# Optimization experiments

Measured on AMD Instinct MI355X. Metric: run time of the kernel, lower is better.

The kernel has to match this reference:

```python
import math
import jax, jax.numpy as jnp
import numpy as np

B, S, HID = 2, 2048, 1024
NH, DQ, DV = 16, 64, 64

def _alibi_bias(n_heads, maxlen):
    # standard ALiBi slopes: 2^(-8*(h+1)/n_heads)
    slopes = jnp.asarray([2.0 ** (-8.0 * (h + 1) / n_heads) for h in range(n_heads)], dtype=jnp.float32)
    pos = jnp.arange(maxlen, dtype=jnp.float32)
    rel = pos[None, :] - pos[:, None]              # [i, j] = j - i  (<= 0 on causal part)
    return slopes[:, None, None] * rel[None]       # [n_heads, maxlen, maxlen]

def setup_inputs() -> dict:
    key = jax.random.key(0)
    ks = jax.random.split(key, 6)
    scale = 0.02
    return {
        "hidden_states": jax.random.normal(ks[0], (B, S, HID), dtype=jnp.float32),
        "attention_mask": jnp.ones((B, S), dtype=jnp.int32),
        "Wq": jax.random.normal(ks[1], (HID, NH * DQ), dtype=jnp.float32) * scale,
        "Wk": jax.random.normal(ks[2], (HID, NH * DQ), dtype=jnp.float32) * scale,
        "Wv": jax.random.normal(ks[3], (HID, NH * DV), dtype=jnp.float32) * scale,
        "Wo": jax.random.normal(ks[4], (NH * DV, HID), dtype=jnp.float32) * scale,
        "bo": jnp.zeros((HID,), dtype=jnp.float32),
        "alibi": _alibi_bias(NH, S),
    }

def reference(hidden_states, attention_mask, Wq, Wk, Wv, Wo, bo, alibi):
    N, t, _ = hidden_states.shape
    # QKV projections (no bias), split into heads: [N, H, t, d]
    q = (hidden_states @ Wq).reshape(N, t, NH, DQ).transpose(0, 2, 1, 3)
    k = (hidden_states @ Wk).reshape(N, t, NH, DQ).transpose(0, 2, 1, 3)
    v = (hidden_states @ Wv).reshape(N, t, NH, DV).transpose(0, 2, 1, 3)
    # raw scores, then ALiBi added BEFORE the 1/sqrt(d) scaling (as in source)
    scores = jnp.einsum("bhid,bhjd->bhij", q, k)
    scores = scores + alibi[None, :, :t, :t]
    scores = scores / math.sqrt(DQ)
    # grok tanh softcap at 30
    scores = 30.0 * jnp.tanh(scores / 30.0)
    # causal + padding masks
    causal = jnp.tril(jnp.ones((t, t), dtype=bool))
    scores = jnp.where(causal[None, None], scores, -jnp.inf)
    pad = (attention_mask != 0)[:, None, None, :]  # [N,1,1,T]
    scores = jnp.where(pad, scores, -jnp.inf)
    probs = jax.nn.softmax(scores, axis=-1)        # dropout p=0.0 (eval)
    ctx = jnp.einsum("bhij,bhjd->bhid", probs, v)
    ctx = ctx.transpose(0, 2, 1, 3).reshape(N, t, NH * DV)
    out = ctx @ Wo + bo
    return out
```

## Files before the change

kernel.cpp:

```cpp
#include <hip/hip_runtime.h>
#include <hip/hip_bf16.h>
#include <stdint.h>

#define BB 2
#define SS 2048
#define HID 1024
#define NHEAD 16
#define DHEAD 64
#define MTOT (BB*SS)

typedef float  f32x4  __attribute__((ext_vector_type(4)));
typedef short  s16x8  __attribute__((ext_vector_type(8)));
typedef unsigned short u16x4 __attribute__((ext_vector_type(4)));

#define LOG2E 1.4426950408889634f

__device__ __forceinline__ unsigned short f2bf(float x){
  union { float f; unsigned u; } v; v.f = x;
  unsigned r = v.u + 0x7fffu + ((v.u >> 16) & 1u);
  return (unsigned short)(r >> 16);
}
__device__ __forceinline__ unsigned pk2bf(float a, float b){
  __hip_bfloat162 h = __float22bfloat162_rn(make_float2(a, b));
  union { __hip_bfloat162 h; unsigned u; } v; v.h = h; return v.u;
}
__device__ __forceinline__ float bf2f(unsigned short h){
  union { unsigned u; float f; } v; v.u = ((unsigned)h) << 16; return v.f;
}

__device__ __forceinline__ void gl2lds16(const unsigned short* g, unsigned short* l){
  __builtin_amdgcn_global_load_lds((const __attribute__((address_space(1))) void*)g,
                                   (__attribute__((address_space(3))) void*)l, 16, 0, 0);
}

__global__ __launch_bounds__(256) void k_convert_x(const float* __restrict__ x,
                                                   unsigned short* __restrict__ xb){
  int i = blockIdx.x * 256 + threadIdx.x;
  const float4* xp = (const float4*)x;
  float4 v = xp[i];
  uint2 o; o.x = pk2bf(v.x, v.y); o.y = pk2bf(v.z, v.w);
  ((uint2*)xb)[i] = o;
}

__global__ __launch_bounds__(256) void k_convert_w(const float* __restrict__ Wq,
                                                   const float* __restrict__ Wk,
                                                   const float* __restrict__ Wv,
                                                   const float* __restrict__ Wo,
                                                   unsigned short* __restrict__ Wt,
                                                   unsigned short* __restrict__ Wot){
  __shared__ float tile[64][65];
  int z = blockIdx.z;
  const float* src = (z==0) ? Wq : (z==1) ? Wk : (z==2) ? Wv : Wo;
  unsigned short* dst = (z < 3) ? (Wt + z * HID * HID) : Wot;
  int n0 = blockIdx.x * 64, k0 = blockIdx.y * 64;
  int t = threadIdx.x, tx = t & 63, ty = t >> 6;
  #pragma unroll
  for (int i = 0; i < 16; i++){
    int kl = ty + i*4;
    tile[kl][tx] = src[(k0 + kl) * HID + n0 + tx];
  }
  __syncthreads();
  #pragma unroll
  for (int i = 0; i < 16; i++){
    int nl = ty + i*4;
    dst[(n0 + nl) * HID + k0 + tx] = f2bf(tile[tx][nl]);
  }
}

__global__ __launch_bounds__(256) void k_gemm_qkv(const unsigned short* __restrict__ A,
                                                  const unsigned short* __restrict__ Bt,
                                                  unsigned short* __restrict__ Qb,
                                                  unsigned short* __restrict__ Kb,
                                                  unsigned short* __restrict__ Vb){
  __shared__ __align__(16) unsigned short As[128*32];
  __shared__ __align__(16) unsigned short Bs[128*32];
  int t = threadIdx.x;
  int L = t & 63, w = t >> 6;
  int q = L >> 4, c = L & 15;
  int id = blockIdx.x;
  int xcd = id & 7, pos = id >> 3;
  int m0 = (xcd*4 + (pos & 3)) * 128;
  int n0 = (pos >> 2) * 128;
  int wr = w >> 1, wc = w & 1;
  f32x4 acc[4][4];
  #pragma unroll
  for (int i = 0; i < 4; i++)
    #pragma unroll
    for (int j = 0; j < 4; j++) acc[i][j] = (f32x4){0.f,0.f,0.f,0.f};

  for (int kb = 0; kb < 32; kb++){
    __syncthreads();
    #pragma unroll
    for (int i = 0; i < 2; i++){
      int p = t + i*256;
      int row = p >> 2, cp = p & 3;
      gl2lds16(A  + (m0 + row) * HID + kb*32 + cp*8, As + p*8);
      gl2lds16(Bt + (n0 + row) * HID + kb*32 + cp*8, Bs + p*8);
    }
    __syncthreads();
    s16x8 af[4], bf[4];
    #pragma unroll
    for (int i = 0; i < 4; i++){
      int m = wr*64 + i*16 + c;
      af[i] = *(const s16x8*)(As + m*32 + q*8);
      int n = wc*64 + i*16 + c;
      bf[i] = *(const s16x8*)(Bs + n*32 + q*8);
    }
    #pragma unroll
    for (int i = 0; i < 4; i++)
      #pragma unroll
      for (int j = 0; j < 4; j++)
        acc[i][j] = __builtin_amdgcn_mfma_f32_16x16x32_bf16(af[i], bf[j], acc[i][j], 0, 0, 0);
  }

  int wsel = n0 >> 10;
  unsigned short* dst = (wsel==0) ? Qb : (wsel==1) ? Kb : Vb;
  float scale = (wsel==0) ? 0.125f : 1.0f;
  #pragma unroll
  for (int i = 0; i < 4; i++){
    #pragma unroll
    for (int j = 0; j < 4; j++){
      int m_l = wr*64 + i*16 + q*4;
      int nw  = (n0 + wc*64 + j*16 + c) & 1023;
      unsigned ua = pk2bf(acc[i][j][0]*scale, acc[i][j][1]*scale);
      unsigned ub = pk2bf(acc[i][j][2]*scale, acc[i][j][3]*scale);
      dst[(m0 + m_l + 0) * HID + nw] = (unsigned short)ua;
      dst[(m0 + m_l + 1) * HID + nw] = (unsigned short)(ua >> 16);
      dst[(m0 + m_l + 2) * HID + nw] = (unsigned short)ub;
      dst[(m0 + m_l + 3) * HID + nw] = (unsigned short)(ub >> 16);
    }
  }
}

__global__ __launch_bounds__(256) void k_transpose_v(const unsigned short* __restrict__ Vb,
                                                     unsigned short* __restrict__ Vt){
  __shared__ unsigned tile[64][33];
  int st = blockIdx.x, bh = blockIdx.y;
  int b = bh >> 4, h = bh & 15;
  int t = threadIdx.x;
  int lr = t >> 4, lc = t & 15;
  #pragma unroll
  for (int i = 0; i < 4; i++){
    int sl = lr + i*16;
    u16x4 v = *(const u16x4*)(Vb + (size_t)(b*SS + st*64 + sl) * HID + h*DHEAD + lc*4);
    tile[sl][lc*2]     = (unsigned)v.x | ((unsigned)v.y << 16);
    tile[sl][lc*2 + 1] = (unsigned)v.z | ((unsigned)v.w << 16);
  }
  __syncthreads();
  #pragma unroll
  for (int i = 0; i < 4; i++){
    int dl = lr + i*16;
    int sh = (dl & 1) * 16, dw = dl >> 1;
    u16x4 o;
    o.x = (unsigned short)(tile[lc*4 + 0][dw] >> sh);
    o.y = (unsigned short)(tile[lc*4 + 1][dw] >> sh);
    o.z = (unsigned short)(tile[lc*4 + 2][dw] >> sh);
    o.w = (unsigned short)(tile[lc*4 + 3][dw] >> sh);
    *(u16x4*)(Vt + (size_t)(bh*DHEAD + dl) * SS + st*64 + lc*4) = o;
  }
}

__global__ __launch_bounds__(256) void k_attn(const unsigned short* __restrict__ Qb,
                                              const unsigned short* __restrict__ Kb,
                                              const unsigned short* __restrict__ Vt,
                                              const int* __restrict__ amask,
                                              unsigned short* __restrict__ NumBf,
                                              float* __restrict__ Lsum,
                                              float* __restrict__ Part2,
                                              float* __restrict__ L2){
  __shared__ __align__(16) unsigned short UQ[4*16*72];
  __shared__ __align__(16) unsigned short Ks[64*64];
  __shared__ __align__(16) unsigned short Vs[64*64];

  int t = threadIdx.x;
  int L = t & 63, w = t >> 6;
  int q = L >> 4, c = L & 15;
  int x = blockIdx.x;
  int bh = blockIdx.y;
  int b = bh >> 4, h = bh & 15;

  int qt, ci, nc;
  if (x < 24){        qt = 31 - x/3;           ci = x % 3;       nc = 3; }
  else if (x < 48){   int y = x - 24; qt = 23 - y/2; ci = y & 1; nc = 2; }
  else {              qt = 59 - x;             ci = 0;           nc = 1; }
  int i0 = qt * 64;

  int hp = h + 1;
  float slope = (hp & 1) ? 0.70710678118654752f : 1.0f;
  slope = ldexpf(slope, -((hp >> 1) + 3));

  int Di = (int)(15.0f / slope);
  int dd = i0 - Di;
  int jt_lo = dd > 0 ? (dd >> 6) : 0;
  int nt = qt + 1 - jt_lo;
  int jt0 = jt_lo + (nt * ci) / nc;
  int jt1 = jt_lo + (nt * (ci + 1)) / nc;

  #pragma unroll
  for (int i = 0; i < 2; i++){
    int p = t + i*256; int row = p >> 3, cp = p & 7; int gc = cp ^ (row & 7);
    gl2lds16(Qb + (size_t)(b*SS + i0 + row) * HID + h*DHEAD + gc*8, UQ + p*8);
  }
  __syncthreads();
  s16x8 qf0, qf1;
  {
    int m = w*16 + c;
    qf0 = *(const s16x8*)(UQ + m*64 + ((0 + q) ^ (m & 7)) * 8);
    qf1 = *(const s16x8*)(UQ + m*64 + ((4 + q) ^ (m & 7)) * 8);
  }

  float si[4];
  #pragma unroll
  for (int r = 0; r < 4; r++) si[r] = slope * (float)(i0 + w*16 + q*4 + r);

  f32x4 cacc[4];
  #pragma unroll
  for (int i = 0; i < 4; i++) cacc[i] = (f32x4){0.f,0.f,0.f,0.f};
  float lrow[4] = {0.f,0.f,0.f,0.f};

  const float C1 = 86.5617024533378f;
  const float C2 = 0.0961796693925976f;

  for (int jt = jt0; jt < jt1; jt++){
    int j0 = jt * 64;
    __syncthreads();
    #pragma unroll
    for (int i = 0; i < 2; i++){
      int p = t + i*256; int row = p >> 3, cp = p & 7; int gc = cp ^ (row & 7);
      gl2lds16(Kb + (size_t)(b*SS + j0 + row) * HID + h*DHEAD + gc*8, Ks + p*8);
      gl2lds16(Vt + (size_t)(bh*DHEAD + row) * SS + j0 + gc*8, Vs + p*8);
    }
    __syncthreads();

    f32x4 sacc[4];
    #pragma unroll
    for (int ct = 0; ct < 4; ct++){
      int n = ct*16 + c;
      s16x8 kf0 = *(const s16x8*)(Ks + n*64 + ((0 + q) ^ (n & 7)) * 8);
      s16x8 kf1 = *(const s16x8*)(Ks + n*64 + ((4 + q) ^ (n & 7)) * 8);
      f32x4 z = (f32x4){0.f,0.f,0.f,0.f};
      z = __builtin_amdgcn_mfma_f32_16x16x32_bf16(qf0, kf0, z, 0, 0, 0);
      z = __builtin_amdgcn_mfma_f32_16x16x32_bf16(qf1, kf1, z, 0, 0, 0);
      sacc[ct] = z;
    }

    float p_[4][4];
    #pragma unroll
    for (int ct = 0; ct < 4; ct++){
      int jg = j0 + ct*16 + c;
      float padf = (amask[b*SS + jg] != 0) ? 1.0f : 0.0f;
      float sjg = slope * (float)jg;
      #pragma unroll
      for (int r = 0; r < 4; r++){
        float s = sacc[ct][r] + (sjg - si[r]);
        float e2 = exp2f(s * C2);
        float pv = exp2f(-C1 * __builtin_amdgcn_rcpf(e2 + 1.0f));
        p_[ct][r] = pv * padf;
      }
    }
    if (jt == qt){
      #pragma unroll
      for (int ct = 0; ct < 4; ct++){
        int jg = j0 + ct*16 + c;
        #pragma unroll
        for (int r = 0; r < 4; r++){
          int ig = i0 + w*16 + q*4 + r;
          if (jg > ig) p_[ct][r] = 0.0f;
        }
      }
    }
    #pragma unroll
    for (int ct = 0; ct < 4; ct++)
      #pragma unroll
      for (int r = 0; r < 4; r++) lrow[r] += p_[ct][r];

    unsigned short* pw = UQ + w * (16*72);
    #pragma unroll
    for (int r = 0; r < 4; r++){
      unsigned ua = pk2bf(p_[0][r], p_[1][r]);
      unsigned ub = pk2bf(p_[2][r], p_[3][r]);
      unsigned short* rowp = pw + (q*4 + r)*72 + c;
      rowp[0]  = (unsigned short)ua;
      rowp[16] = (unsigned short)(ua >> 16);
      rowp[32] = (unsigned short)ub;
      rowp[48] = (unsigned short)(ub >> 16);
    }

    s16x8 pf0 = *(const s16x8*)(pw + c*72 + q*8);
    s16x8 pf1 = *(const s16x8*)(pw + c*72 + 32 + q*8);
    #pragma unroll
    for (int nt_ = 0; nt_ < 4; nt_++){
      int d = nt_*16 + c;
      s16x8 vf0 = *(const s16x8*)(Vs + d*64 + ((0 + q) ^ (d & 7)) * 8);
      s16x8 vf1 = *(const s16x8*)(Vs + d*64 + ((4 + q) ^ (d & 7)) * 8);
      cacc[nt_] = __builtin_amdgcn_mfma_f32_16x16x32_bf16(pf0, vf0, cacc[nt_], 0, 0, 0);
      cacc[nt_] = __builtin_amdgcn_mfma_f32_16x16x32_bf16(pf1, vf1, cacc[nt_], 0, 0, 0);
    }
  }

  float lred[4];
  #pragma unroll
  for (int r = 0; r < 4; r++){
    float l = lrow[r];
    l += __shfl_xor(l, 1, 64);
    l += __shfl_xor(l, 2, 64);
    l += __shfl_xor(l, 4, 64);
    l += __shfl_xor(l, 8, 64);
    lred[r] = l;
  }

  if (ci == 0){
    #pragma unroll
    for (int r = 0; r < 4; r++){
      int ig = i0 + w*16 + q*4 + r;
      unsigned short* rowp = NumBf + (size_t)(b*SS + ig) * HID + h*DHEAD + c;
      unsigned ua = pk2bf(cacc[0][r], cacc[1][r]);
      unsigned ub = pk2bf(cacc[2][r], cacc[3][r]);
      rowp[0]  = (unsigned short)ua;
      rowp[16] = (unsigned short)(ua >> 16);
      rowp[32] = (unsigned short)ub;
      rowp[48] = (unsigned short)(ub >> 16);
    }
    if (c == 0){
      #pragma unroll
      for (int r = 0; r < 4; r++)
        Lsum[bh*SS + i0 + w*16 + q*4 + r] = lred[r];
    }
  } else {
    int local = (qt < 24) ? (qt - 12) : (12 + (qt - 24)*2 + (ci - 1));
    int slot = bh*28 + local;
    float* pn = Part2 + (size_t)slot * 64 * 64;
    #pragma unroll
    for (int nt_ = 0; nt_ < 4; nt_++){
      int d = nt_*16 + c;
      #pragma unroll
      for (int r = 0; r < 4; r++){
        int row = w*16 + q*4 + r;
        pn[row*64 + d] = cacc[nt_][r];
      }
    }
    if (c == 0){
      #pragma unroll
      for (int r = 0; r < 4; r++)
        L2[slot*64 + w*16 + q*4 + r] = lred[r];
    }
  }
}

__global__ __launch_bounds__(256) void k_combine(unsigned short* __restrict__ NumBf,
                                                 const float* __restrict__ Lsum,
                                                 const float* __restrict__ Part2,
                                                 const float* __restrict__ L2){
  int idx = blockIdx.x * 256 + threadIdx.x;
  int tok = idx >> 8;
  int hd4 = (idx & 255) * 4;
  int h = hd4 >> 6, d0 = hd4 & 63;
  int b = tok >> 11, i = tok & 2047;
  int bh = b*16 + h, qt = i >> 6;
  u16x4 nv = *(u16x4*)(NumBf + (size_t)tok * HID + hd4);
  float n0 = bf2f(nv.x), n1 = bf2f(nv.y), n2 = bf2f(nv.z), n3 = bf2f(nv.w);
  float l = Lsum[bh*SS + i];
  int nparts = (qt >= 24) ? 2 : (qt >= 12 ? 1 : 0);
  if (nparts > 0){
    int local = (qt < 24) ? (qt - 12) : (12 + (qt - 24)*2);
    int slot = bh*28 + local;
    for (int pi = 0; pi < nparts; pi++){
      const float* pn = Part2 + ((size_t)(slot + pi) * 64 + (i & 63)) * 64 + d0;
      n0 += pn[0]; n1 += pn[1]; n2 += pn[2]; n3 += pn[3];
      l += L2[(slot + pi)*64 + (i & 63)];
    }
  }
  float rl = __builtin_amdgcn_rcpf(l);
  uint2 o; o.x = pk2bf(n0*rl, n1*rl); o.y = pk2bf(n2*rl, n3*rl);
  *(uint2*)(NumBf + (size_t)tok * HID + hd4) = o;
}

__global__ __launch_bounds__(256) void k_gemm_out(const unsigned short* __restrict__ A,
                                                  const unsigned short* __restrict__ Bt,
                                                  float* __restrict__ out,
                                                  const float* __restrict__ bo){
  __shared__ __align__(16) unsigned short As[64*32];
  __shared__ __align__(16) unsigned short Bs[128*32];
  int t = threadIdx.x;
  int L = t & 63, w = t >> 6;
  int q = L >> 4, c = L & 15;
  int id = blockIdx.x;
  int xcd = id & 7, pos = id >> 3;
  int m0 = (xcd*8 + (pos & 7)) * 64;
  int n0 = (pos >> 3) * 128;
  int wr = w >> 1, wc = w & 1;
  f32x4 acc[2][4];
  #pragma unroll
  for (int i = 0; i < 2; i++)
    #pragma unroll
    for (int j = 0; j < 4; j++) acc[i][j] = (f32x4){0.f,0.f,0.f,0.f};

  for (int kb = 0; kb < 32; kb++){
    __syncthreads();
    {
      int row = t >> 2, cp = t & 3;
      gl2lds16(A + (m0 + row) * HID + kb*32 + cp*8, As + t*8);
    }
    #pragma unroll
    for (int i = 0; i < 2; i++){
      int p = t + i*256;
      int row = p >> 2, cp = p & 3;
      gl2lds16(Bt + (n0 + row) * HID + kb*32 + cp*8, Bs + p*8);
    }
    __syncthreads();
    s16x8 af[2], bf[4];
    #pragma unroll
    for (int i = 0; i < 2; i++){
      int m = wr*32 + i*16 + c;
      af[i] = *(const s16x8*)(As + m*32 + q*8);
    }
    #pragma unroll
    for (int j = 0; j < 4; j++){
      int n = wc*64 + j*16 + c;
      bf[j] = *(const s16x8*)(Bs + n*32 + q*8);
    }
    #pragma unroll
    for (int i = 0; i < 2; i++)
      #pragma unroll
      for (int j = 0; j < 4; j++)
        acc[i][j] = __builtin_amdgcn_mfma_f32_16x16x32_bf16(af[i], bf[j], acc[i][j], 0, 0, 0);
  }

  #pragma unroll
  for (int j = 0; j < 4; j++){
    int n = n0 + wc*64 + j*16 + c;
    float bv = bo[n];
    #pragma unroll
    for (int i = 0; i < 2; i++){
      int m = m0 + wr*32 + i*16 + q*4;
      #pragma unroll
      for (int r = 0; r < 4; r++)
        out[(size_t)(m + r) * HID + n] = acc[i][j][r] + bv;
    }
  }
}

extern "C" void kernel_launch(void* const* d_in, const int* in_sizes, int n_in,
                              void* d_out, int out_size, void* d_ws, size_t ws_size,
                              hipStream_t stream){
  const float* hs    = (const float*)d_in[0];
  const int*   amask = (const int*)  d_in[1];
  const float* Wq    = (const float*)d_in[2];
  const float* Wk    = (const float*)d_in[3];
  const float* Wv    = (const float*)d_in[4];
  const float* Wo    = (const float*)d_in[5];
  const float* bo    = (const float*)d_in[6];
  float* out = (float*)d_out;

  char* ws = (char*)d_ws;
  unsigned short* Xb  = (unsigned short*)(ws);
  unsigned short* Wt  = (unsigned short*)(ws + (8u  << 20));
  unsigned short* Wot = (unsigned short*)(ws + (14u << 20));
  unsigned short* Qb  = (unsigned short*)(ws + (16u << 20));
  unsigned short* Kb  = (unsigned short*)(ws + (24u << 20));
  unsigned short* Vt  = (unsigned short*)(ws + (32u << 20));
  unsigned short* Ctx = (unsigned short*)(ws + (40u << 20));
  float* Part2 = (float*)(ws + (48u << 20));
  float* L2    = (float*)(ws + (63u << 20));
  float* Lsum  = (float*)(ws + (63u << 20) + (512u << 10));
  unsigned short* Vb = Ctx;

  hipLaunchKernelGGL(k_convert_x,  dim3(MTOT*HID/4/256), dim3(256), 0, stream, hs, Xb);
  hipLaunchKernelGGL(k_convert_w,  dim3(16,16,4), dim3(256), 0, stream, Wq, Wk, Wv, Wo, Wt, Wot);
  hipLaunchKernelGGL(k_gemm_qkv,   dim3(768),     dim3(256), 0, stream, Xb, Wt, Qb, Kb, Vb);
  hipLaunchKernelGGL(k_transpose_v,dim3(32,32),   dim3(256), 0, stream, Vb, Vt);
  hipLaunchKernelGGL(k_attn,       dim3(60,32),   dim3(256), 0, stream, Qb, Kb, Vt, amask,
                                   Ctx, Lsum, Part2, L2);
  hipLaunchKernelGGL(k_combine,    dim3(MTOT*HID/4/256), dim3(256), 0, stream, Ctx, Lsum, Part2, L2);
  hipLaunchKernelGGL(k_gemm_out,   dim3(512),     dim3(256), 0, stream, Ctx, Wot, out, bo);
}
```

Baseline: 450.1 us.

## Load Q/K/V MFMA fragments directly from global memory, drop LDS staging

The attention kernel no longer stages Q, K and V tiles through shared memory with block-wide barriers. Each wave now loads its MFMA operand fragments straight from global memory into registers, and only the per-wave P tile stays in LDS. This removes the __syncthreads pairs and LDS round trips per key tile. In exchange, each of the four waves fetches the same K/V tile separately, which raises global/L2 traffic and register pressure, and the latency of those loads is exposed without a prefetch.

After: 510.8 us. 1.13x slower.

```diff
diff --git a/kernel.cpp b/kernel.cpp
--- a/kernel.cpp
+++ b/kernel.cpp
@@ -168,9 +168,7 @@
                                               float* __restrict__ Lsum,
                                               float* __restrict__ Part2,
                                               float* __restrict__ L2){
-  __shared__ __align__(16) unsigned short UQ[4*16*72];
-  __shared__ __align__(16) unsigned short Ks[64*64];
-  __shared__ __align__(16) unsigned short Vs[64*64];
+  __shared__ __align__(16) unsigned short Ps[4][16*72];
 
   int t = threadIdx.x;
   int L = t & 63, w = t >> 6;
@@ -192,22 +190,13 @@
   int Di = (int)(15.0f / slope);
   int dd = i0 - Di;
   int jt_lo = dd > 0 ? (dd >> 6) : 0;
-  int nt = qt + 1 - jt_lo;
-  int jt0 = jt_lo + (nt * ci) / nc;
-  int jt1 = jt_lo + (nt * (ci + 1)) / nc;
-
-  #pragma unroll
-  for (int i = 0; i < 2; i++){
-    int p = t + i*256; int row = p >> 3, cp = p & 7; int gc = cp ^ (row & 7);
-    gl2lds16(Qb + (size_t)(b*SS + i0 + row) * HID + h*DHEAD + gc*8, UQ + p*8);
-  }
-  __syncthreads();
-  s16x8 qf0, qf1;
-  {
-    int m = w*16 + c;
-    qf0 = *(const s16x8*)(UQ + m*64 + ((0 + q) ^ (m & 7)) * 8);
-    qf1 = *(const s16x8*)(UQ + m*64 + ((4 + q) ^ (m & 7)) * 8);
-  }
+  int ntl = qt + 1 - jt_lo;
+  int jt0 = jt_lo + (ntl * ci) / nc;
+  int jt1 = jt_lo + (ntl * (ci + 1)) / nc;
+
+  const unsigned short* qptr = Qb + (size_t)(b*SS + i0 + w*16 + c) * HID + h*DHEAD + q*8;
+  s16x8 qf0 = *(const s16x8*)(qptr);
+  s16x8 qf1 = *(const s16x8*)(qptr + 32);
 
   float si[4];
   #pragma unroll
@@ -221,26 +210,32 @@
   const float C1 = 86.5617024533378f;
   const float C2 = 0.0961796693925976f;
 
+  unsigned short* pw = &Ps[w][0];
+
   for (int jt = jt0; jt < jt1; jt++){
     int j0 = jt * 64;
-    __syncthreads();
-    #pragma unroll
-    for (int i = 0; i < 2; i++){
-      int p = t + i*256; int row = p >> 3, cp = p & 7; int gc = cp ^ (row & 7);
-      gl2lds16(Kb + (size_t)(b*SS + j0 + row) * HID + h*DHEAD + gc*8, Ks + p*8);
-      gl2lds16(Vt + (size_t)(bh*DHEAD + row) * SS + j0 + gc*8, Vs + p*8);
-    }
-    __syncthreads();
+
+    const unsigned short* kbase = Kb + (size_t)(b*SS + j0 + c) * HID + h*DHEAD + q*8;
+    s16x8 kf0[4], kf1[4];
+    #pragma unroll
+    for (int ct = 0; ct < 4; ct++){
+      kf0[ct] = *(const s16x8*)(kbase + (size_t)(ct*16) * HID);
+      kf1[ct] = *(const s16x8*)(kbase + (size_t)(ct*16) * HID + 32);
+    }
+    const unsigned short* vbase = Vt + (size_t)(bh*DHEAD + c) * SS + j0 + q*8;
+    s16x8 vf0[4], vf1[4];
+    #pragma unroll
+    for (int nt_ = 0; nt_ < 4; nt_++){
+      vf0[nt_] = *(const s16x8*)(vbase + (size_t)(nt_*16) * SS);
+      vf1[nt_] = *(const s16x8*)(vbase + (size_t)(nt_*16) * SS + 32);
+    }
 
     f32x4 sacc[4];
     #pragma unroll
     for (int ct = 0; ct < 4; ct++){
-      int n = ct*16 + c;
-      s16x8 kf0 = *(const s16x8*)(Ks + n*64 + ((0 + q) ^ (n & 7)) * 8);
-      s16x8 kf1 = *(const s16x8*)(Ks + n*64 + ((4 + q) ^ (n & 7)) * 8);
       f32x4 z = (f32x4){0.f,0.f,0.f,0.f};
-      z = __builtin_amdgcn_mfma_f32_16x16x32_bf16(qf0, kf0, z, 0, 0, 0);
-      z = __builtin_amdgcn_mfma_f32_16x16x32_bf16(qf1, kf1, z, 0, 0, 0);
+      z = __builtin_amdgcn_mfma_f32_16x16x32_bf16(qf0, kf0[ct], z, 0, 0, 0);
+      z = __builtin_amdgcn_mfma_f32_16x16x32_bf16(qf1, kf1[ct], z, 0, 0, 0);
       sacc[ct] = z;
     }
 
@@ -274,7 +269,6 @@
       #pragma unroll
       for (int r = 0; r < 4; r++) lrow[r] += p_[ct][r];
 
-    unsigned short* pw = UQ + w * (16*72);
     #pragma unroll
     for (int r = 0; r < 4; r++){
       unsigned ua = pk2bf(p_[0][r], p_[1][r]);
@@ -290,11 +284,8 @@
     s16x8 pf1 = *(const s16x8*)(pw + c*72 + 32 + q*8);
     #pragma unroll
     for (int nt_ = 0; nt_ < 4; nt_++){
-      int d = nt_*16 + c;
-      s16x8 vf0 = *(const s16x8*)(Vs + d*64 + ((0 + q) ^ (d & 7)) * 8);
-      s16x8 vf1 = *(const s16x8*)(Vs + d*64 + ((4 + q) ^ (d & 7)) * 8);
-      cacc[nt_] = __builtin_amdgcn_mfma_f32_16x16x32_bf16(pf0, vf0, cacc[nt_], 0, 0, 0);
-      cacc[nt_] = __builtin_amdgcn_mfma_f32_16x16x32_bf16(pf1, vf1, cacc[nt_], 0, 0, 0);
+      cacc[nt_] = __builtin_amdgcn_mfma_f32_16x16x32_bf16(pf0, vf0[nt_], cacc[nt_], 0, 0, 0);
+      cacc[nt_] = __builtin_amdgcn_mfma_f32_16x16x32_bf16(pf1, vf1[nt_], cacc[nt_], 0, 0, 0);
     }
   }
 
```
